# Kernel tuning notes

Measured on AMD Instinct MI355X. Metric: run time of the kernel, lower is better.

Reference implementation:

```python
import jax, jax.numpy as jnp
import numpy as np

N, D_IN, H, E, L = 8192, 512, 256, 262144, 2
LN_EPS = 1e-5


def _unique_edges(rng, n, e):
    # sample unique (src,tgt) pairs so scatter-set semantics are well-defined
    flat = np.unique(rng.integers(0, n * n, size=int(e * 1.2)))
    rng.shuffle(flat)
    flat = flat[:e]
    assert flat.shape[0] == e
    return np.stack([flat // n, flat % n]).astype(np.int64)


def setup_inputs() -> dict:
    key = jax.random.key(0)
    ks = jax.random.split(key, 8)
    rng = np.random.default_rng(0)
    inv = lambda fan: 1.0 / np.sqrt(fan)
    return {
        "node_features": jax.random.normal(ks[0], (N, D_IN), jnp.float32),
        "edge_index": jnp.asarray(_unique_edges(rng, N, E)),
        "W_in": jax.random.uniform(ks[1], (H, D_IN), jnp.float32, -inv(D_IN), inv(D_IN)),
        "b_in": jnp.zeros((H,), jnp.float32),
        "W_gat": jax.random.uniform(ks[2], (L, H, H), jnp.float32, -inv(H), inv(H)),
        "a_gat": jax.random.uniform(ks[3], (L, 2 * H), jnp.float32, -inv(2 * H), inv(2 * H)),
        "ln_g": jnp.ones((L, H), jnp.float32),
        "ln_b": jnp.zeros((L, H), jnp.float32),
        "W_pool": jax.random.uniform(ks[4], (1, H), jnp.float32, -inv(H), inv(H)),
        "b_pool": jnp.zeros((1,), jnp.float32),
    }


def _layer_norm(x, g, b):
    mu = x.mean(-1, keepdims=True)
    var = ((x - mu) ** 2).mean(-1, keepdims=True)
    return (x - mu) * jax.lax.rsqrt(var + LN_EPS) * g + b


def reference(node_features, edge_index, W_in, b_in, W_gat, a_gat, ln_g, ln_b, W_pool, b_pool):
    src, tgt = edge_index[0], edge_index[1]
    n = node_features.shape[0]
    h = node_features @ W_in.T + b_in  # (N, H)
    nl = W_gat.shape[0]
    for l in range(nl):
        hw = h @ W_gat[l].T  # (N, H)
        # attention score per edge: attn([h_src || h_tgt]) with LeakyReLU(0.2)
        e = hw[src] @ a_gat[l, :H] + hw[tgt] @ a_gat[l, H:]  # (E,)
        e = jnp.where(e > 0, e, 0.2 * e)
        # faithful to torch: dense NxN with zeros at non-edges, full-row softmax
        alpha = jnp.zeros((n, n), h.dtype).at[src, tgt].set(e)
        alpha = jax.nn.softmax(alpha, axis=-1)
        h_new = alpha @ hw  # (N, H)  (dropout is eval-mode identity)
        h = _layer_norm(h + h_new, ln_g[l], ln_b[l])
        h = jax.nn.elu(h)
    gate = jax.nn.sigmoid(h @ W_pool.T + b_pool)  # (N, 1)
    graph_emb = (gate * h).sum(axis=0)  # (H,)
    return h, graph_emb
```

## Files before the change

kernel.cpp:

```cpp
#include <hip/hip_runtime.h>
#include <hip/hip_bf16.h>
#include <stdint.h>

#define NN 8192
#define DIN 512
#define HH 256
#define EE 262144
#define LN_EPS 1e-5f

typedef __attribute__((ext_vector_type(8))) short bf16x8;
typedef __attribute__((ext_vector_type(4))) short s16x4;
typedef __attribute__((ext_vector_type(4))) float f32x4;

__device__ __forceinline__ short f2bf_bits(float x) {
    __hip_bfloat16 b = __float2bfloat16(x);
    return __builtin_bit_cast(short, b);
}
__device__ __forceinline__ float bf2f(short s) {
    uint32_t u = ((uint32_t)(uint16_t)s) << 16;
    return __builtin_bit_cast(float, u);
}

__global__ __launch_bounds__(256) void f2b2(const float* __restrict__ x1, __hip_bfloat16* __restrict__ y1, int n1,
                                            const float* __restrict__ x2, __hip_bfloat16* __restrict__ y2, int n2) {
    int base = (blockIdx.x * 256 + threadIdx.x) * 4;
    const float* x; __hip_bfloat16* y; int b;
    if (base < n1) { x = x1; y = y1; b = base; }
    else { b = base - n1; if (b >= n2) return; x = x2; y = y2; }
    float4 v = *(const float4*)(x + b);
    y[b + 0] = __float2bfloat16(v.x);
    y[b + 1] = __float2bfloat16(v.y);
    y[b + 2] = __float2bfloat16(v.z);
    y[b + 3] = __float2bfloat16(v.w);
}

__global__ void count_edges(const int* __restrict__ src, int* __restrict__ cnt) {
    int k = blockIdx.x * 256 + threadIdx.x;
    if (k < EE) atomicAdd(&cnt[src[k]], 1);
}

__global__ __launch_bounds__(1024) void scan_deg(const int* __restrict__ deg, int* __restrict__ row_start) {
    __shared__ int sums[1024];
    int t = threadIdx.x;
    int base = t * 8;
    int loc[8];
    int s = 0;
#pragma unroll
    for (int i = 0; i < 8; i++) { loc[i] = s; s += deg[base + i]; }
    sums[t] = s;
    __syncthreads();
    for (int off = 1; off < 1024; off <<= 1) {
        int v = (t >= off) ? sums[t - off] : 0;
        __syncthreads();
        sums[t] += v;
        __syncthreads();
    }
    int excl = (t == 0) ? 0 : sums[t - 1];
#pragma unroll
    for (int i = 0; i < 8; i++) row_start[base + i] = excl + loc[i];
    if (t == 1023) row_start[NN] = sums[1023];
}

__global__ void fill_edges(const int* __restrict__ src, const int* __restrict__ tgt,
                           const int* __restrict__ row_start, int* __restrict__ cnt,
                           int* __restrict__ col) {
    int k = blockIdx.x * 256 + threadIdx.x;
    if (k < EE) {
        int s = src[k];
        int p = row_start[s] + atomicAdd(&cnt[s], 1);
        col[p] = tgt[k];
    }
}

__device__ __forceinline__ void load16_lds(const void* g, void* l) {
    __builtin_amdgcn_global_load_lds((const __attribute__((address_space(1))) uint32_t*)g,
                                     (__attribute__((address_space(3))) uint32_t*)l, 16, 0, 0);
}

__global__ __launch_bounds__(256) void gemm_f32a(const float* __restrict__ A,
                                                 const __hip_bfloat16* __restrict__ B,
                                                 const float* __restrict__ bias,
                                                 __hip_bfloat16* __restrict__ Cb,
                                                 int M, int Nc, int K) {
    __shared__ __hip_bfloat16 As[64 * 32];
    __shared__ __hip_bfloat16 Bs[64 * 32];
    const int tid = threadIdx.x;
    const int row0 = blockIdx.y * 64, col0 = blockIdx.x * 64;
    const int w = tid >> 6, l = tid & 63;
    const int quad = l >> 4, r = l & 15;
    const int mh = (w & 1) * 32, nh = (w >> 1) * 32;
    f32x4 acc[2][2] = {};

    const int srow = tid >> 2, scol = (tid & 3) * 8;
    const float* gA = A + (size_t)(row0 + srow) * K + scol;
    const __hip_bfloat16* gB = B + (size_t)(col0 + srow) * K + scol;
    __hip_bfloat16* lB = &Bs[tid * 8];
    __hip_bfloat16* lA = &As[tid * 8];

    for (int k0 = 0; k0 < K; k0 += 32) {
        load16_lds(gB + k0, lB);
        float4 a0 = *(const float4*)(gA + k0);
        float4 a1 = *(const float4*)(gA + k0 + 4);
        bf16x8 av;
        av[0] = f2bf_bits(a0.x); av[1] = f2bf_bits(a0.y);
        av[2] = f2bf_bits(a0.z); av[3] = f2bf_bits(a0.w);
        av[4] = f2bf_bits(a1.x); av[5] = f2bf_bits(a1.y);
        av[6] = f2bf_bits(a1.z); av[7] = f2bf_bits(a1.w);
        *(bf16x8*)lA = av;
        __syncthreads();
        bf16x8 aF[2], bF[2];
#pragma unroll
        for (int mi = 0; mi < 2; mi++)
            aF[mi] = *(const bf16x8*)&As[(mh + mi * 16 + r) * 32 + quad * 8];
#pragma unroll
        for (int ni = 0; ni < 2; ni++)
            bF[ni] = *(const bf16x8*)&Bs[(nh + ni * 16 + r) * 32 + quad * 8];
#pragma unroll
        for (int mi = 0; mi < 2; mi++)
#pragma unroll
            for (int ni = 0; ni < 2; ni++)
                acc[mi][ni] = __builtin_amdgcn_mfma_f32_16x16x32_bf16(aF[mi], bF[ni], acc[mi][ni], 0, 0, 0);
        __syncthreads();
    }

#pragma unroll
    for (int mi = 0; mi < 2; mi++)
#pragma unroll
        for (int ni = 0; ni < 2; ni++) {
            int gcol = col0 + nh + ni * 16 + r;
            float bv = bias[gcol];
#pragma unroll
            for (int reg = 0; reg < 4; reg++) {
                int grow = row0 + mh + mi * 16 + quad * 4 + reg;
                Cb[(size_t)grow * Nc + gcol] = __float2bfloat16(acc[mi][ni][reg] + bv);
            }
        }
}

__global__ __launch_bounds__(256) void gemm_bb_score(const __hip_bfloat16* __restrict__ A,
                                                     const __hip_bfloat16* __restrict__ B,
                                                     __hip_bfloat16* __restrict__ Cb,
                                                     const float* __restrict__ ag1,
                                                     const float* __restrict__ ag2,
                                                     float* __restrict__ s1, float* __restrict__ s2,
                                                     float* __restrict__ St,
                                                     int M, int Nc, int K) {
    __shared__ __hip_bfloat16 As[64 * 32];
    __shared__ __hip_bfloat16 Bs[64 * 32];
    const int tid = threadIdx.x;
    const int row0 = blockIdx.y * 64, col0 = blockIdx.x * 64;
    const int w = tid >> 6, l = tid & 63;
    const int quad = l >> 4, r = l & 15;
    const int mh = (w & 1) * 32, nh = (w >> 1) * 32;
    f32x4 acc[2][2] = {};

    const int srow = tid >> 2, scol = (tid & 3) * 8;
    const __hip_bfloat16* gA = A + (size_t)(row0 + srow) * K + scol;
    const __hip_bfloat16* gB = B + (size_t)(col0 + srow) * K + scol;
    __hip_bfloat16* lA = &As[tid * 8];
    __hip_bfloat16* lB = &Bs[tid * 8];

    for (int k0 = 0; k0 < K; k0 += 32) {
        load16_lds(gA + k0, lA);
        load16_lds(gB + k0, lB);
        __syncthreads();
        bf16x8 aF[2], bF[2];
#pragma unroll
        for (int mi = 0; mi < 2; mi++)
            aF[mi] = *(const bf16x8*)&As[(mh + mi * 16 + r) * 32 + quad * 8];
#pragma unroll
        for (int ni = 0; ni < 2; ni++)
            bF[ni] = *(const bf16x8*)&Bs[(nh + ni * 16 + r) * 32 + quad * 8];
#pragma unroll
        for (int mi = 0; mi < 2; mi++)
#pragma unroll
            for (int ni = 0; ni < 2; ni++)
                acc[mi][ni] = __builtin_amdgcn_mfma_f32_16x16x32_bf16(aF[mi], bF[ni], acc[mi][ni], 0, 0, 0);
        __syncthreads();
    }

#pragma unroll
    for (int mi = 0; mi < 2; mi++)
#pragma unroll
        for (int ni = 0; ni < 2; ni++) {
            int gcol = col0 + nh + ni * 16 + r;
#pragma unroll
            for (int reg = 0; reg < 4; reg++) {
                int grow = row0 + mh + mi * 16 + quad * 4 + reg;
                Cb[(size_t)grow * Nc + gcol] = __float2bfloat16(acc[mi][ni][reg]);
            }
        }

    float a1v[2], a2v[2];
#pragma unroll
    for (int ni = 0; ni < 2; ni++) {
        int gcol = col0 + nh + ni * 16 + r;
        a1v[ni] = ag1[gcol];
        a2v[ni] = ag2[gcol];
    }
#pragma unroll
    for (int mi = 0; mi < 2; mi++)
#pragma unroll
        for (int reg = 0; reg < 4; reg++) {
            float p1 = acc[mi][0][reg] * a1v[0] + acc[mi][1][reg] * a1v[1];
            float p2 = acc[mi][0][reg] * a2v[0] + acc[mi][1][reg] * a2v[1];
#pragma unroll
            for (int off = 1; off <= 8; off <<= 1) {
                p1 += __shfl_xor(p1, off);
                p2 += __shfl_xor(p2, off);
            }
            if (r == 0) {
                int grow = row0 + mh + mi * 16 + quad * 4 + reg;
                atomicAdd(&s1[grow], p1);
                atomicAdd(&s2[grow], p2);
            }
        }
#pragma unroll
    for (int ni = 0; ni < 2; ni++) {
        float pS = 0.f;
#pragma unroll
        for (int mi = 0; mi < 2; mi++)
#pragma unroll
            for (int reg = 0; reg < 4; reg++) pS += acc[mi][ni][reg];
        pS += __shfl_xor(pS, 16);
        pS += __shfl_xor(pS, 32);
        if (quad == 0) atomicAdd(&St[col0 + nh + ni * 16 + r], pS);
    }
}

__global__ __launch_bounds__(256) void gat_row(const __hip_bfloat16* __restrict__ hprev,
                                               const __hip_bfloat16* __restrict__ hw,
                                               const int* __restrict__ row_start, const int* __restrict__ col_idx,
                                               const float* __restrict__ s1, const float* __restrict__ s2,
                                               const float* __restrict__ St,
                                               const float* __restrict__ lng, const float* __restrict__ lnb,
                                               const float* __restrict__ W_pool, const float* __restrict__ b_pool,
                                               float* __restrict__ houtf, __hip_bfloat16* __restrict__ houtb,
                                               float* __restrict__ gate, int last) {
    const int wv = threadIdx.x >> 6, lane = threadIdx.x & 63;
    const int i = blockIdx.x * 4 + wv;
    const int beg = row_start[i], end = row_start[i + 1];
    const int deg = end - beg;
    const float s1i = s1[i];

    float lmax = 0.f;
    for (int k = beg + lane; k < end; k += 64) {
        float e = s1i + s2[col_idx[k]];
        e = e > 0.f ? e : 0.2f * e;
        lmax = fmaxf(lmax, e);
    }
#pragma unroll
    for (int off = 32; off; off >>= 1) lmax = fmaxf(lmax, __shfl_xor(lmax, off));
    const float m = lmax;

    float lsum = 0.f;
    for (int k = beg + lane; k < end; k += 64) {
        float e = s1i + s2[col_idx[k]];
        e = e > 0.f ? e : 0.2f * e;
        lsum += __expf(e - m);
    }
#pragma unroll
    for (int off = 32; off; off >>= 1) lsum += __shfl_xor(lsum, off);

    const float em = __expf(-m);
    const float Z = (float)(NN - deg) * em + lsum;
    const float invZ = 1.f / Z;
    const float c = em * invZ;

    const float4 Stv = *(const float4*)(St + 4 * lane);
    float ac0 = c * Stv.x, ac1 = c * Stv.y, ac2 = c * Stv.z, ac3 = c * Stv.w;
    const short* hws = (const short*)hw;

    for (int kb = beg; kb < end; kb += 64) {
        int k = kb + lane;
        float wk = 0.f;
        int ck = 0;
        if (k < end) {
            int j = col_idx[k];
            float e = s1i + s2[j];
            e = e > 0.f ? e : 0.2f * e;
            wk = __expf(e - m) * invZ - c;
            ck = j;
        }
        int nb = min(64, end - kb);
#pragma unroll 4
        for (int jj = 0; jj < nb; jj++) {
            float wj = __shfl(wk, jj);
            int cj = __shfl(ck, jj);
            s16x4 hv = *(const s16x4*)(hws + (size_t)cj * HH + 4 * lane);
            ac0 += wj * bf2f(hv[0]);
            ac1 += wj * bf2f(hv[1]);
            ac2 += wj * bf2f(hv[2]);
            ac3 += wj * bf2f(hv[3]);
        }
    }

    s16x4 hp = *(const s16x4*)((const short*)hprev + (size_t)i * HH + 4 * lane);
    float x0 = bf2f(hp[0]) + ac0;
    float x1 = bf2f(hp[1]) + ac1;
    float x2 = bf2f(hp[2]) + ac2;
    float x3 = bf2f(hp[3]) + ac3;
    float ssum = x0 + x1 + x2 + x3;
#pragma unroll
    for (int off = 32; off; off >>= 1) ssum += __shfl_xor(ssum, off);
    float mu = ssum * (1.f / HH);
    float d0 = x0 - mu, d1 = x1 - mu, d2 = x2 - mu, d3 = x3 - mu;
    float vsum = d0 * d0 + d1 * d1 + d2 * d2 + d3 * d3;
#pragma unroll
    for (int off = 32; off; off >>= 1) vsum += __shfl_xor(vsum, off);
    float rstd = rsqrtf(vsum * (1.f / HH) + LN_EPS);
    float4 g4 = *(const float4*)(lng + 4 * lane);
    float4 b4 = *(const float4*)(lnb + 4 * lane);
    float y0 = d0 * rstd * g4.x + b4.x;
    float y1 = d1 * rstd * g4.y + b4.y;
    float y2 = d2 * rstd * g4.z + b4.z;
    float y3 = d3 * rstd * g4.w + b4.w;
    y0 = y0 > 0.f ? y0 : __expf(y0) - 1.f;
    y1 = y1 > 0.f ? y1 : __expf(y1) - 1.f;
    y2 = y2 > 0.f ? y2 : __expf(y2) - 1.f;
    y3 = y3 > 0.f ? y3 : __expf(y3) - 1.f;

    s16x4 yv;
    yv[0] = f2bf_bits(y0); yv[1] = f2bf_bits(y1); yv[2] = f2bf_bits(y2); yv[3] = f2bf_bits(y3);
    *(s16x4*)((short*)houtb + (size_t)i * HH + 4 * lane) = yv;
    if (houtf) {
        float4 yf = { y0, y1, y2, y3 };
        *(float4*)(houtf + (size_t)i * HH + 4 * lane) = yf;
    }

    if (last) {
        float4 wp = *(const float4*)(W_pool + 4 * lane);
        float p = y0 * wp.x + y1 * wp.y + y2 * wp.z + y3 * wp.w;
#pragma unroll
        for (int off = 32; off; off >>= 1) p += __shfl_xor(p, off);
        if (lane == 0) {
            float g = p + b_pool[0];
            gate[i] = 1.f / (1.f + __expf(-g));
        }
    }
}

__global__ __launch_bounds__(256) void pool_kernel(const float* __restrict__ h, const float* __restrict__ gate,
                                                   float* __restrict__ emb) {
    int c = threadIdx.x;
    int r0 = blockIdx.x * 32;
    float acc = 0.f;
#pragma unroll
    for (int rr = 0; rr < 32; rr++) {
        int r = r0 + rr;
        acc += gate[r] * h[(size_t)r * HH + c];
    }
    atomicAdd(&emb[c], acc);
}

extern "C" void kernel_launch(void* const* d_in, const int* in_sizes, int n_in,
                              void* d_out, int out_size, void* d_ws, size_t ws_size,
                              hipStream_t stream) {
    const float* X      = (const float*)d_in[0];
    const int*   ei     = (const int*)d_in[1];
    const float* W_in   = (const float*)d_in[2];
    const float* b_in   = (const float*)d_in[3];
    const float* W_gat  = (const float*)d_in[4];
    const float* a_gat  = (const float*)d_in[5];
    const float* ln_g   = (const float*)d_in[6];
    const float* ln_b   = (const float*)d_in[7];
    const float* W_pool = (const float*)d_in[8];
    const float* b_pool = (const float*)d_in[9];
    float* out = (float*)d_out;

    __hip_bfloat16* hb    = (__hip_bfloat16*)d_ws;
    __hip_bfloat16* hwb   = hb + (size_t)NN * HH;
    __hip_bfloat16* Wb_in = hwb + (size_t)NN * HH;
    __hip_bfloat16* Wgb   = Wb_in + (size_t)HH * DIN;
    float* zbase = (float*)(Wgb + (size_t)2 * HH * HH);
    float* s1_0 = zbase;
    float* s2_0 = s1_0 + NN;
    float* St_0 = s2_0 + NN;
    float* s1_1 = St_0 + HH;
    float* s2_1 = s1_1 + NN;
    float* St_1 = s2_1 + NN;
    int* cnt  = (int*)(St_1 + HH);
    int* cnt2 = cnt + NN;
    size_t zcount = (size_t)2 * (2 * NN + HH) + 2 * NN;
    float* gate = (float*)(cnt2 + NN);
    int* row_start = (int*)(gate + NN);
    int* col = row_start + NN + 1;

    const int* src = ei;
    const int* tgt = ei + EE;

    hipMemsetAsync(zbase, 0, zcount * 4, stream);

    f2b2<<<(HH * DIN + 2 * HH * HH) / 1024, 256, 0, stream>>>(W_in, Wb_in, HH * DIN, W_gat, Wgb, 2 * HH * HH);

    count_edges<<<EE / 256, 256, 0, stream>>>(src, cnt);
    scan_deg<<<1, 1024, 0, stream>>>(cnt, row_start);
    fill_edges<<<EE / 256, 256, 0, stream>>>(src, tgt, row_start, cnt2, col);

    gemm_f32a<<<dim3(HH / 64, NN / 64), 256, 0, stream>>>(X, Wb_in, b_in, hb, NN, HH, DIN);

    for (int ll = 0; ll < 2; ll++) {
        float* s1 = ll ? s1_1 : s1_0;
        float* s2 = ll ? s2_1 : s2_0;
        float* St = ll ? St_1 : St_0;
        const float* ag = a_gat + (size_t)ll * 2 * HH;
        gemm_bb_score<<<dim3(HH / 64, NN / 64), 256, 0, stream>>>(hb, Wgb + (size_t)ll * HH * HH, hwb,
                                                                  ag, ag + HH, s1, s2, St, NN, HH, HH);
        gat_row<<<NN / 4, 256, 0, stream>>>(hb, hwb, row_start, col, s1, s2, St,
                                            ln_g + (size_t)ll * HH, ln_b + (size_t)ll * HH,
                                            W_pool, b_pool,
                                            (ll == 1) ? out : nullptr, hb, gate, ll);
    }

    hipMemsetAsync(out + (size_t)NN * HH, 0, HH * sizeof(float), stream);
    pool_kernel<<<NN / 32, 256, 0, stream>>>(out, gate, out + (size_t)NN * HH);
}
```

Baseline: 208.0 us.

## Fuse whole GAT pipeline into one cooperative persistent kernel with grid syncs

Replaces the sequence of about eleven launches and memsets (weight conversion, CSR build, input GEMM, per-layer score GEMM and row aggregation, pooling) with a single cooperative kernel of 512 blocks separated by grid.sync barriers. The CSR fill now runs in the same phase as the first GEMM tile, so that work overlaps. The aim is to remove launch gaps and per-kernel ramp-up on a pipeline that is short overall. In exchange, the degree scan runs on only one block while the rest wait, each grid sync costs time, and occupancy is capped at two blocks per CU.

New measurement: 706.0 us. 239% more time.

```diff
diff --git a/kernel.cpp b/kernel.cpp
--- a/kernel.cpp
+++ b/kernel.cpp
@@ -1,12 +1,17 @@
 #include <hip/hip_runtime.h>
+#include <hip/hip_cooperative_groups.h>
 #include <hip/hip_bf16.h>
 #include <stdint.h>
+
+namespace cg = cooperative_groups;
 
 #define NN 8192
 #define DIN 512
 #define HH 256
 #define EE 262144
 #define LN_EPS 1e-5f
+#define GRID 512
+#define NTHREADS (GRID * 256)
 
 typedef __attribute__((ext_vector_type(8))) short bf16x8;
 typedef __attribute__((ext_vector_type(4))) short s16x4;
@@ -20,84 +25,28 @@
     uint32_t u = ((uint32_t)(uint16_t)s) << 16;
     return __builtin_bit_cast(float, u);
 }
-
-__global__ __launch_bounds__(256) void f2b2(const float* __restrict__ x1, __hip_bfloat16* __restrict__ y1, int n1,
-                                            const float* __restrict__ x2, __hip_bfloat16* __restrict__ y2, int n2) {
-    int base = (blockIdx.x * 256 + threadIdx.x) * 4;
-    const float* x; __hip_bfloat16* y; int b;
-    if (base < n1) { x = x1; y = y1; b = base; }
-    else { b = base - n1; if (b >= n2) return; x = x2; y = y2; }
-    float4 v = *(const float4*)(x + b);
-    y[b + 0] = __float2bfloat16(v.x);
-    y[b + 1] = __float2bfloat16(v.y);
-    y[b + 2] = __float2bfloat16(v.z);
-    y[b + 3] = __float2bfloat16(v.w);
-}
-
-__global__ void count_edges(const int* __restrict__ src, int* __restrict__ cnt) {
-    int k = blockIdx.x * 256 + threadIdx.x;
-    if (k < EE) atomicAdd(&cnt[src[k]], 1);
-}
-
-__global__ __launch_bounds__(1024) void scan_deg(const int* __restrict__ deg, int* __restrict__ row_start) {
-    __shared__ int sums[1024];
-    int t = threadIdx.x;
-    int base = t * 8;
-    int loc[8];
-    int s = 0;
-#pragma unroll
-    for (int i = 0; i < 8; i++) { loc[i] = s; s += deg[base + i]; }
-    sums[t] = s;
-    __syncthreads();
-    for (int off = 1; off < 1024; off <<= 1) {
-        int v = (t >= off) ? sums[t - off] : 0;
-        __syncthreads();
-        sums[t] += v;
-        __syncthreads();
-    }
-    int excl = (t == 0) ? 0 : sums[t - 1];
-#pragma unroll
-    for (int i = 0; i < 8; i++) row_start[base + i] = excl + loc[i];
-    if (t == 1023) row_start[NN] = sums[1023];
-}
-
-__global__ void fill_edges(const int* __restrict__ src, const int* __restrict__ tgt,
-                           const int* __restrict__ row_start, int* __restrict__ cnt,
-                           int* __restrict__ col) {
-    int k = blockIdx.x * 256 + threadIdx.x;
-    if (k < EE) {
-        int s = src[k];
-        int p = row_start[s] + atomicAdd(&cnt[s], 1);
-        col[p] = tgt[k];
-    }
-}
-
 __device__ __forceinline__ void load16_lds(const void* g, void* l) {
     __builtin_amdgcn_global_load_lds((const __attribute__((address_space(1))) uint32_t*)g,
                                      (__attribute__((address_space(3))) uint32_t*)l, 16, 0, 0);
 }
 
-__global__ __launch_bounds__(256) void gemm_f32a(const float* __restrict__ A,
-                                                 const __hip_bfloat16* __restrict__ B,
-                                                 const float* __restrict__ bias,
-                                                 __hip_bfloat16* __restrict__ Cb,
-                                                 int M, int Nc, int K) {
-    __shared__ __hip_bfloat16 As[64 * 32];
-    __shared__ __hip_bfloat16 Bs[64 * 32];
+__device__ void gemm1_tile(int b, const float* __restrict__ A, const __hip_bfloat16* __restrict__ B,
+                           const float* __restrict__ bias, __hip_bfloat16* __restrict__ Cb,
+                           __hip_bfloat16* As, __hip_bfloat16* Bs) {
     const int tid = threadIdx.x;
-    const int row0 = blockIdx.y * 64, col0 = blockIdx.x * 64;
+    const int row0 = (b >> 2) * 64, col0 = (b & 3) * 64;
     const int w = tid >> 6, l = tid & 63;
     const int quad = l >> 4, r = l & 15;
     const int mh = (w & 1) * 32, nh = (w >> 1) * 32;
     f32x4 acc[2][2] = {};
 
     const int srow = tid >> 2, scol = (tid & 3) * 8;
-    const float* gA = A + (size_t)(row0 + srow) * K + scol;
-    const __hip_bfloat16* gB = B + (size_t)(col0 + srow) * K + scol;
+    const float* gA = A + (size_t)(row0 + srow) * DIN + scol;
+    const __hip_bfloat16* gB = B + (size_t)(col0 + srow) * DIN + scol;
     __hip_bfloat16* lB = &Bs[tid * 8];
     __hip_bfloat16* lA = &As[tid * 8];
 
-    for (int k0 = 0; k0 < K; k0 += 32) {
+    for (int k0 = 0; k0 < DIN; k0 += 32) {
         load16_lds(gB + k0, lB);
         float4 a0 = *(const float4*)(gA + k0);
         float4 a1 = *(const float4*)(gA + k0 + 4);
@@ -132,35 +81,30 @@
 #pragma unroll
             for (int reg = 0; reg < 4; reg++) {
                 int grow = row0 + mh + mi * 16 + quad * 4 + reg;
-                Cb[(size_t)grow * Nc + gcol] = __float2bfloat16(acc[mi][ni][reg] + bv);
+                Cb[(size_t)grow * HH + gcol] = __float2bfloat16(acc[mi][ni][reg] + bv);
             }
         }
 }
 
-__global__ __launch_bounds__(256) void gemm_bb_score(const __hip_bfloat16* __restrict__ A,
-                                                     const __hip_bfloat16* __restrict__ B,
-                                                     __hip_bfloat16* __restrict__ Cb,
-                                                     const float* __restrict__ ag1,
-                                                     const float* __restrict__ ag2,
-                                                     float* __restrict__ s1, float* __restrict__ s2,
-                                                     float* __restrict__ St,
-                                                     int M, int Nc, int K) {
-    __shared__ __hip_bfloat16 As[64 * 32];
-    __shared__ __hip_bfloat16 Bs[64 * 32];
+__device__ void gemm2_tile(int b, const __hip_bfloat16* __restrict__ A, const __hip_bfloat16* __restrict__ B,
+                           __hip_bfloat16* __restrict__ Cb,
+                           const float* __restrict__ ag1, const float* __restrict__ ag2,
+                           float* __restrict__ s1, float* __restrict__ s2, float* __restrict__ St,
+                           __hip_bfloat16* As, __hip_bfloat16* Bs) {
     const int tid = threadIdx.x;
-    const int row0 = blockIdx.y * 64, col0 = blockIdx.x * 64;
+    const int row0 = (b >> 2) * 64, col0 = (b & 3) * 64;
     const int w = tid >> 6, l = tid & 63;
     const int quad = l >> 4, r = l & 15;
     const int mh = (w & 1) * 32, nh = (w >> 1) * 32;
     f32x4 acc[2][2] = {};
 
     const int srow = tid >> 2, scol = (tid & 3) * 8;
-    const __hip_bfloat16* gA = A + (size_t)(row0 + srow) * K + scol;
-    const __hip_bfloat16* gB = B + (size_t)(col0 + srow) * K + scol;
+    const __hip_bfloat16* gA = A + (size_t)(row0 + srow) * HH + scol;
+    const __hip_bfloat16* gB = B + (size_t)(col0 + srow) * HH + scol;
     __hip_bfloat16* lA = &As[tid * 8];
     __hip_bfloat16* lB = &Bs[tid * 8];
 
-    for (int k0 = 0; k0 < K; k0 += 32) {
+    for (int k0 = 0; k0 < HH; k0 += 32) {
         load16_lds(gA + k0, lA);
         load16_lds(gB + k0, lB);
         __syncthreads();
@@ -187,7 +131,7 @@
 #pragma unroll
             for (int reg = 0; reg < 4; reg++) {
                 int grow = row0 + mh + mi * 16 + quad * 4 + reg;
-                Cb[(size_t)grow * Nc + gcol] = __float2bfloat16(acc[mi][ni][reg]);
+                Cb[(size_t)grow * HH + gcol] = __float2bfloat16(acc[mi][ni][reg]);
             }
         }
 
@@ -228,17 +172,15 @@
     }
 }
 
-__global__ __launch_bounds__(256) void gat_row(const __hip_bfloat16* __restrict__ hprev,
-                                               const __hip_bfloat16* __restrict__ hw,
-                                               const int* __restrict__ row_start, const int* __restrict__ col_idx,
-                                               const float* __restrict__ s1, const float* __restrict__ s2,
-                                               const float* __restrict__ St,
-                                               const float* __restrict__ lng, const float* __restrict__ lnb,
-                                               const float* __restrict__ W_pool, const float* __restrict__ b_pool,
-                                               float* __restrict__ houtf, __hip_bfloat16* __restrict__ houtb,
-                                               float* __restrict__ gate, int last) {
-    const int wv = threadIdx.x >> 6, lane = threadIdx.x & 63;
-    const int i = blockIdx.x * 4 + wv;
+__device__ void gat_row_dev(int i, int lane,
+                            const __hip_bfloat16* hprev, const __hip_bfloat16* __restrict__ hw,
+                            const int* __restrict__ row_start, const int* __restrict__ col_idx,
+                            const float* __restrict__ s1, const float* __restrict__ s2,
+                            const float* __restrict__ St,
+                            const float* __restrict__ lng, const float* __restrict__ lnb,
+                            const float* __restrict__ W_pool, const float* __restrict__ b_pool,
+                            float* houtf, __hip_bfloat16* houtb,
+                            float* __restrict__ gate, int last) {
     const int beg = row_start[i], end = row_start[i + 1];
     const int deg = end - beg;
     const float s1i = s1[i];
@@ -340,17 +282,124 @@
     }
 }
 
-__global__ __launch_bounds__(256) void pool_kernel(const float* __restrict__ h, const float* __restrict__ gate,
-                                                   float* __restrict__ emb) {
-    int c = threadIdx.x;
-    int r0 = blockIdx.x * 32;
-    float acc = 0.f;
-#pragma unroll
-    for (int rr = 0; rr < 32; rr++) {
-        int r = r0 + rr;
-        acc += gate[r] * h[(size_t)r * HH + c];
-    }
-    atomicAdd(&emb[c], acc);
+__global__ __launch_bounds__(256, 2) void mono(
+    const float* X, const int* ei,
+    const float* W_in, const float* b_in,
+    const float* W_gat, const float* a_gat,
+    const float* ln_g, const float* ln_b,
+    const float* W_pool, const float* b_pool,
+    __hip_bfloat16* hb, __hip_bfloat16* hwb,
+    __hip_bfloat16* Wb_in, __hip_bfloat16* Wgb,
+    float* zbase, float* out) {
+    __shared__ __hip_bfloat16 sAs[64 * 32];
+    __shared__ __hip_bfloat16 sBs[64 * 32];
+    __shared__ int sScan[256];
+
+    cg::grid_group grid = cg::this_grid();
+
+    float* s1_0 = zbase;
+    float* s2_0 = s1_0 + NN;
+    float* St_0 = s2_0 + NN;
+    float* s1_1 = St_0 + HH;
+    float* s2_1 = s1_1 + NN;
+    float* St_1 = s2_1 + NN;
+    int* cnt  = (int*)(St_1 + HH);
+    int* cnt2 = cnt + NN;
+    float* gate = (float*)(cnt2 + NN);
+    int* row_start = (int*)(gate + NN);
+    int* col = row_start + NN + 1;
+    float* emb = out + (size_t)NN * HH;
+    const int* src = ei;
+    const int* tgt = ei + EE;
+
+    const int tid = threadIdx.x;
+    const int gtid = blockIdx.x * 256 + tid;
+    const int wv = tid >> 6, lane = tid & 63;
+    const int ZCOUNT = 2 * (2 * NN + HH) + 2 * NN;
+
+    {
+        int* zi = (int*)zbase;
+        if (gtid < ZCOUNT) zi[gtid] = 0;
+        if (gtid < HH) emb[gtid] = 0.f;
+        const int n1 = HH * DIN, n2 = 2 * HH * HH;
+        int q = gtid;
+        if (q < (n1 + n2) / 4) {
+            int base = q * 4;
+            const float* x;
+            __hip_bfloat16* y;
+            int bidx;
+            if (base < n1) { x = W_in; y = Wb_in; bidx = base; }
+            else { x = W_gat; y = Wgb; bidx = base - n1; }
+            float4 v = *(const float4*)(x + bidx);
+            y[bidx + 0] = __float2bfloat16(v.x);
+            y[bidx + 1] = __float2bfloat16(v.y);
+            y[bidx + 2] = __float2bfloat16(v.z);
+            y[bidx + 3] = __float2bfloat16(v.w);
+        }
+    }
+    grid.sync();
+
+    for (int k = gtid; k < EE; k += NTHREADS) atomicAdd(&cnt[src[k]], 1);
+    grid.sync();
+
+    if (blockIdx.x == 0) {
+        int base = tid * 32;
+        int lsum = 0;
+        for (int i2 = 0; i2 < 32; i2++) lsum += cnt[base + i2];
+        sScan[tid] = lsum;
+        __syncthreads();
+        for (int off = 1; off < 256; off <<= 1) {
+            int v = (tid >= off) ? sScan[tid - off] : 0;
+            __syncthreads();
+            sScan[tid] += v;
+            __syncthreads();
+        }
+        int excl = (tid == 0) ? 0 : sScan[tid - 1];
+        for (int i2 = 0; i2 < 32; i2++) { row_start[base + i2] = excl; excl += cnt[base + i2]; }
+        if (tid == 255) row_start[NN] = EE;
+    }
+    grid.sync();
+
+    for (int k = gtid; k < EE; k += NTHREADS) {
+        int s = src[k];
+        int p = row_start[s] + atomicAdd(&cnt2[s], 1);
+        col[p] = tgt[k];
+    }
+    gemm1_tile(blockIdx.x, X, Wb_in, b_in, hb, sAs, sBs);
+    grid.sync();
+
+    gemm2_tile(blockIdx.x, hb, Wgb, hwb, a_gat, a_gat + HH, s1_0, s2_0, St_0, sAs, sBs);
+    grid.sync();
+
+    for (int rg = blockIdx.x; rg < NN / 4; rg += GRID) {
+        int i = rg * 4 + wv;
+        gat_row_dev(i, lane, hb, hwb, row_start, col, s1_0, s2_0, St_0,
+                    ln_g, ln_b, W_pool, b_pool, nullptr, hb, gate, 0);
+    }
+    grid.sync();
+
+    gemm2_tile(blockIdx.x, hb, Wgb + (size_t)HH * HH, hwb,
+               a_gat + 2 * HH, a_gat + 3 * HH, s1_1, s2_1, St_1, sAs, sBs);
+    grid.sync();
+
+    for (int rg = blockIdx.x; rg < NN / 4; rg += GRID) {
+        int i = rg * 4 + wv;
+        gat_row_dev(i, lane, hb, hwb, row_start, col, s1_1, s2_1, St_1,
+                    ln_g + HH, ln_b + HH, W_pool, b_pool, out, hb, gate, 1);
+    }
+    grid.sync();
+
+    if (blockIdx.x < 256) {
+        int c = tid;
+        int r0 = blockIdx.x * 32;
+        float acc = 0.f;
+#pragma unroll
+        for (int rr = 0; rr < 32; rr++) {
+            int r = r0 + rr;
+            acc += gate[r] * out[(size_t)r * HH + c];
+        }
+        atomicAdd(&emb[c], acc);
+    }
 }
 
 extern "C" void kernel_launch(void* const* d_in, const int* in_sizes, int n_in,
@@ -373,45 +422,11 @@
     __hip_bfloat16* Wb_in = hwb + (size_t)NN * HH;
     __hip_bfloat16* Wgb   = Wb_in + (size_t)HH * DIN;
     float* zbase = (float*)(Wgb + (size_t)2 * HH * HH);
-    float* s1_0 = zbase;
-    float* s2_0 = s1_0 + NN;
-    float* St_0 = s2_0 + NN;
-    float* s1_1 = St_0 + HH;
-    float* s2_1 = s1_1 + NN;
-    float* St_1 = s2_1 + NN;
-    int* cnt  = (int*)(St_1 + HH);
-    int* cnt2 = cnt + NN;
-    size_t zcount = (size_t)2 * (2 * NN + HH) + 2 * NN;
-    float* gate = (float*)(cnt2 + NN);
-    int* row_start = (int*)(gate + NN);
-    int* col = row_start + NN + 1;
-
-    const int* src = ei;
-    const int* tgt = ei + EE;
-
-    hipMemsetAsync(zbase, 0, zcount * 4, stream);
-
-    f2b2<<<(HH * DIN + 2 * HH * HH) / 1024, 256, 0, stream>>>(W_in, Wb_in, HH * DIN, W_gat, Wgb, 2 * HH * HH);
-
-    count_edges<<<EE / 256, 256, 0, stream>>>(src, cnt);
-    scan_deg<<<1, 1024, 0, stream>>>(cnt, row_start);
-    fill_edges<<<EE / 256, 256, 0, stream>>>(src, tgt, row_start, cnt2, col);
-
-    gemm_f32a<<<dim3(HH / 64, NN / 64), 256, 0, stream>>>(X, Wb_in, b_in, hb, NN, HH, DIN);
-
-    for (int ll = 0; ll < 2; ll++) {
-        float* s1 = ll ? s1_1 : s1_0;
-        float* s2 = ll ? s2_1 : s2_0;
-        float* St = ll ? St_1 : St_0;
-        const float* ag = a_gat + (size_t)ll * 2 * HH;
-        gemm_bb_score<<<dim3(HH / 64, NN / 64), 256, 0, stream>>>(hb, Wgb + (size_t)ll * HH * HH, hwb,
-                                                                  ag, ag + HH, s1, s2, St, NN, HH, HH);
-        gat_row<<<NN / 4, 256, 0, stream>>>(hb, hwb, row_start, col, s1, s2, St,
-                                            ln_g + (size_t)ll * HH, ln_b + (size_t)ll * HH,
-                                            W_pool, b_pool,
-                                            (ll == 1) ? out : nullptr, hb, gate, ll);
-    }
-
-    hipMemsetAsync(out + (size_t)NN * HH, 0, HH * sizeof(float), stream);
-    pool_kernel<<<NN / 32, 256, 0, stream>>>(out, gate, out + (size_t)NN * HH);
-}
+
+    void* args[] = {
+        (void*)&X, (void*)&ei, (void*)&W_in, (void*)&b_in, (void*)&W_gat, (void*)&a_gat,
+        (void*)&ln_g, (void*)&ln_b, (void*)&W_pool, (void*)&b_pool,
+        (void*)&hb, (void*)&hwb, (void*)&Wb_in, (void*)&Wgb, (void*)&zbase, (void*)&out
+    };
+    (void)hipLaunchCooperativeKernel((void*)mono, dim3(GRID), dim3(256), args, 0, stream);
+}
```
